# Kernel optimization log

Hardware: AMD Instinct MI355X
Metric: run time of the kernel (lower is better)

## Reference

```python
import jax, jax.numpy as jnp
import numpy as np

D_MODEL = 1024
D_FF = 4 * D_MODEL
NUM_EXPERTS = 8
TOP_K = 2
TOKENS = 4096


def setup_inputs() -> dict:
    key = jax.random.key(0)
    ks = jax.random.split(key, 8)
    s = 0.02
    x = jax.random.normal(ks[0], (TOKENS, D_MODEL), dtype=jnp.float32)
    Wg = jax.random.normal(ks[1], (D_MODEL, NUM_EXPERTS), dtype=jnp.float32) * s
    bg = jnp.zeros((NUM_EXPERTS,), dtype=jnp.float32)
    W1 = jax.random.normal(ks[2], (NUM_EXPERTS, D_MODEL, D_FF), dtype=jnp.float32) * s
    b1 = jnp.zeros((NUM_EXPERTS, D_FF), dtype=jnp.float32)
    W2 = jax.random.normal(ks[3], (NUM_EXPERTS, D_FF, D_MODEL), dtype=jnp.float32) * s
    b2 = jnp.zeros((NUM_EXPERTS, D_MODEL), dtype=jnp.float32)
    return {"x": x, "Wg": Wg, "bg": bg, "W1": W1, "b1": b1, "W2": W2, "b2": b2}


def reference(x, Wg, bg, W1, b1, W2, b2):
    # Gating: softmax over experts, select top-k indices per token.
    gate_scores = jax.nn.softmax(x @ Wg + bg, axis=-1)        # [T, E]
    _, top_k_idx = jax.lax.top_k(gate_scores, TOP_K)          # [T, K]
    # Binary combine mask: 1 where expert selected (top_k indices are distinct).
    # NOTE: original sums selected expert outputs WITHOUT gate weighting.
    mask = jnp.sum(jax.nn.one_hot(top_k_idx, NUM_EXPERTS, dtype=x.dtype), axis=1)  # [T, E]
    out = jnp.zeros_like(x)
    for e in range(NUM_EXPERTS):  # small fixed expert count
        h = jax.nn.relu(x @ W1[e] + b1[e])                    # [T, 4D]
        y = h @ W2[e] + b2[e]                                 # [T, D]
        out = out + mask[:, e:e + 1] * y
    return out
```

## Files before the change

kernel.cpp:

```cpp
#include <hip/hip_runtime.h>
#include <hip/hip_bf16.h>

#define T_TOKENS 4096
#define DM 1024
#define DF 4096
#define NE 8
#define MAXROWS 9216

typedef float f32x4 __attribute__((ext_vector_type(4)));
typedef short bf16x8 __attribute__((ext_vector_type(8)));

__device__ __forceinline__ unsigned short f2bf(float f) {
    union { float f; unsigned int u; } v; v.f = f;
    unsigned int r = v.u + 0x7fffu + ((v.u >> 16) & 1u);
    return (unsigned short)(r >> 16);
}

__device__ __forceinline__ void g2l16(const void* g, void* l) {
    __builtin_amdgcn_global_load_lds(
        (const __attribute__((address_space(1))) void*)g,
        (__attribute__((address_space(3))) void*)l, 16, 0, 0);
}

__global__ __launch_bounds__(256) void gate_kernel(
    const float* __restrict__ x, const float* __restrict__ Wg, const float* __restrict__ bg,
    int* __restrict__ counts, int* __restrict__ topk)
{
    int wave = threadIdx.x >> 6;
    int lane = threadIdx.x & 63;
    int t = blockIdx.x * 4 + wave;
    float acc[NE];
#pragma unroll
    for (int e = 0; e < NE; e++) acc[e] = 0.f;
    const float* xr = x + (size_t)t * DM;
#pragma unroll
    for (int i = 0; i < DM / 64; i++) {
        int d = lane + i * 64;
        float xv = xr[d];
        const float4* wg = (const float4*)(Wg + d * NE);
        float4 w0 = wg[0], w1 = wg[1];
        acc[0] += xv * w0.x; acc[1] += xv * w0.y; acc[2] += xv * w0.z; acc[3] += xv * w0.w;
        acc[4] += xv * w1.x; acc[5] += xv * w1.y; acc[6] += xv * w1.z; acc[7] += xv * w1.w;
    }
#pragma unroll
    for (int e = 0; e < NE; e++) {
#pragma unroll
        for (int off = 32; off > 0; off >>= 1)
            acc[e] += __shfl_down(acc[e], off);
    }
    if (lane == 0) {
        float lg[NE];
#pragma unroll
        for (int e = 0; e < NE; e++) lg[e] = acc[e] + bg[e];
        int b1i = 0; float b1v = lg[0];
        for (int e = 1; e < NE; e++) if (lg[e] > b1v) { b1v = lg[e]; b1i = e; }
        int b2i = -1; float b2v = -1e30f;
        for (int e = 0; e < NE; e++) {
            if (e == b1i) continue;
            if (b2i < 0 || lg[e] > b2v) { b2v = lg[e]; b2i = e; }
        }
        topk[t * 2 + 0] = b1i;
        topk[t * 2 + 1] = b2i;
        atomicAdd(&counts[b1i], 1);
        atomicAdd(&counts[b2i], 1);
    }
}

__global__ __launch_bounds__(256) void scatter_kernel(
    const int* __restrict__ counts, const int* __restrict__ topk,
    int* __restrict__ offsets, int* __restrict__ list)
{
    __shared__ int offs[NE + 1];
    __shared__ int cur[NE];
    if (threadIdx.x == 0) {
        int s = 0;
        for (int e = 0; e < NE; e++) {
            offs[e] = s; offsets[e] = s;
            s += (counts[e] + 127) & ~127;
        }
        offs[NE] = s; offsets[NE] = s;
    }
    if (threadIdx.x < NE) cur[threadIdx.x] = 0;
    __syncthreads();
    for (int i = threadIdx.x; i < T_TOKENS * 2; i += 256) {
        int e = topk[i];
        int pos = atomicAdd(&cur[e], 1);
        list[offs[e] + pos] = i >> 1;
    }
    __syncthreads();
    for (int e = 0; e < NE; e++) {
        int s = offs[e] + counts[e];
        int t = offs[e + 1];
        for (int i = s + threadIdx.x; i < t; i += 256) list[i] = -1;
    }
}

__global__ __launch_bounds__(256) void cvt_x_kernel(
    const float* __restrict__ x, unsigned short* __restrict__ xb)
{
    int i = (blockIdx.x * 256 + threadIdx.x) * 4;
    float4 v = *(const float4*)(x + i);
    unsigned short o[4] = { f2bf(v.x), f2bf(v.y), f2bf(v.z), f2bf(v.w) };
    *(uint2*)(xb + i) = *(const uint2*)o;
}

__global__ __launch_bounds__(256) void tr_cvt_kernel(
    const float* __restrict__ src, unsigned short* __restrict__ dst, int K, int N)
{
    const int e = blockIdx.z;
    src += (size_t)e * K * N;
    dst += (size_t)e * N * K;
    const int n0 = blockIdx.x * 64, k0 = blockIdx.y * 64;
    __shared__ unsigned short tile[64][68];
    const int t = threadIdx.x;
    const int tx = t & 63, ty = t >> 6;
#pragma unroll
    for (int r = 0; r < 16; r++) {
        int k = ty * 16 + r;
        tile[tx][k] = f2bf(src[(size_t)(k0 + k) * N + n0 + tx]);
    }
    __syncthreads();
    const int kx = (t & 15) * 4, ny = t >> 4;
#pragma unroll
    for (int r = 0; r < 4; r++) {
        int n = ny + r * 16;
        *(uint2*)(dst + (size_t)(n0 + n) * K + k0 + kx) = *(const uint2*)&tile[n][kx];
    }
}

__global__ __launch_bounds__(256) void gemm1_kernel(
    const unsigned short* __restrict__ xb, const unsigned short* __restrict__ W1T,
    const float* __restrict__ b1, const int* __restrict__ offsets,
    const int* __restrict__ list, unsigned short* __restrict__ H)
{
    const int total = offsets[NE];
    const int row0 = blockIdx.x * 128;
    if (row0 >= total) return;
    int e = 0;
    while (row0 >= offsets[e + 1]) e++;
    const int n0 = blockIdx.y * 128;

    __shared__ unsigned short Asm[128 * 32];
    __shared__ unsigned short Bsm[128 * 32];

    const int tid = threadIdx.x;
    const int w = tid >> 6, lane = tid & 63;
    const int quad = lane >> 4, l16 = lane & 15;
    const int wm = w >> 1, wn = w & 1;

    const int sr = lane >> 2;
    const int sc = (lane & 3) * 8;
    const int ra1 = 32 * w + sr, ra2 = ra1 + 16;
    int t1 = list[row0 + ra1]; if (t1 < 0) t1 = 0;
    int t2 = list[row0 + ra2]; if (t2 < 0) t2 = 0;
    const unsigned short* gA1 = xb + (size_t)t1 * DM + sc;
    const unsigned short* gA2 = xb + (size_t)t2 * DM + sc;
    const unsigned short* Wb = W1T + (size_t)e * DF * DM;
    const unsigned short* gB1 = Wb + (size_t)(n0 + 32 * w + sr) * DM + sc;
    const unsigned short* gB2 = gB1 + (size_t)16 * DM;
    unsigned short* lA1 = Asm + (2 * w) * 512;
    unsigned short* lA2 = Asm + (2 * w + 1) * 512;
    unsigned short* lB1 = Bsm + (2 * w) * 512;
    unsigned short* lB2 = Bsm + (2 * w + 1) * 512;

    f32x4 acc[4][4];
#pragma unroll
    for (int i = 0; i < 4; i++)
#pragma unroll
        for (int j = 0; j < 4; j++) acc[i][j] = (f32x4){0.f, 0.f, 0.f, 0.f};

    for (int kk = 0; kk < DM; kk += 32) {
        g2l16(gA1 + kk, lA1);
        g2l16(gA2 + kk, lA2);
        g2l16(gB1 + kk, lB1);
        g2l16(gB2 + kk, lB2);
        __syncthreads();
        bf16x8 af[4];
#pragma unroll
        for (int i = 0; i < 4; i++)
            af[i] = *(const bf16x8*)&Asm[(wm * 64 + i * 16 + l16) * 32 + quad * 8];
#pragma unroll
        for (int j = 0; j < 4; j++) {
            bf16x8 bf = *(const bf16x8*)&Bsm[(wn * 64 + j * 16 + l16) * 32 + quad * 8];
#pragma unroll
            for (int i = 0; i < 4; i++)
                acc[i][j] = __builtin_amdgcn_mfma_f32_16x16x32_bf16(af[i], bf, acc[i][j], 0, 0, 0);
        }
        __syncthreads();
    }

    const float* bias = b1 + e * DF;
#pragma unroll
    for (int j = 0; j < 4; j++) {
        int n = n0 + wn * 64 + j * 16 + l16;
        float bj = bias[n];
#pragma unroll
        for (int i = 0; i < 4; i++) {
            int row = row0 + wm * 64 + i * 16 + quad * 4;
#pragma unroll
            for (int r = 0; r < 4; r++) {
                float v = acc[i][j][r] + bj;
                v = fmaxf(v, 0.f);
                H[(size_t)(row + r) * DF + n] = f2bf(v);
            }
        }
    }
}

__global__ __launch_bounds__(256) void gemm2_kernel(
    const unsigned short* __restrict__ H, const unsigned short* __restrict__ W2T,
    const float* __restrict__ b2, const int* __restrict__ offsets,
    const int* __restrict__ list, float* __restrict__ out)
{
    const int total = offsets[NE];
    const int row0 = blockIdx.x * 128;
    if (row0 >= total) return;
    int e = 0;
    while (row0 >= offsets[e + 1]) e++;
    const int n0 = blockIdx.y * 128;

    __shared__ unsigned short Asm[128 * 32];
    __shared__ unsigned short Bsm[128 * 32];

    const int tid = threadIdx.x;
    const int w = tid >> 6, lane = tid & 63;
    const int quad = lane >> 4, l16 = lane & 15;
    const int wm = w >> 1, wn = w & 1;

    const int sr = lane >> 2;
    const int sc = (lane & 3) * 8;
    const unsigned short* gA1 = H + (size_t)(row0 + 32 * w + sr) * DF + sc;
    const unsigned short* gA2 = gA1 + (size_t)16 * DF;
    const unsigned short* Wb = W2T + (size_t)e * DM * DF;
    const unsigned short* gB1 = Wb + (size_t)(n0 + 32 * w + sr) * DF + sc;
    const unsigned short* gB2 = gB1 + (size_t)16 * DF;
    unsigned short* lA1 = Asm + (2 * w) * 512;
    unsigned short* lA2 = Asm + (2 * w + 1) * 512;
    unsigned short* lB1 = Bsm + (2 * w) * 512;
    unsigned short* lB2 = Bsm + (2 * w + 1) * 512;

    f32x4 acc[4][4];
#pragma unroll
    for (int i = 0; i < 4; i++)
#pragma unroll
        for (int j = 0; j < 4; j++) acc[i][j] = (f32x4){0.f, 0.f, 0.f, 0.f};

    for (int kk = 0; kk < DF; kk += 32) {
        g2l16(gA1 + kk, lA1);
        g2l16(gA2 + kk, lA2);
        g2l16(gB1 + kk, lB1);
        g2l16(gB2 + kk, lB2);
        __syncthreads();
        bf16x8 af[4];
#pragma unroll
        for (int i = 0; i < 4; i++)
            af[i] = *(const bf16x8*)&Asm[(wm * 64 + i * 16 + l16) * 32 + quad * 8];
#pragma unroll
        for (int j = 0; j < 4; j++) {
            bf16x8 bf = *(const bf16x8*)&Bsm[(wn * 64 + j * 16 + l16) * 32 + quad * 8];
#pragma unroll
            for (int i = 0; i < 4; i++)
                acc[i][j] = __builtin_amdgcn_mfma_f32_16x16x32_bf16(af[i], bf, acc[i][j], 0, 0, 0);
        }
        __syncthreads();
    }

    const float* bias = b2 + e * DM;
#pragma unroll
    for (int j = 0; j < 4; j++) {
        int n = n0 + wn * 64 + j * 16 + l16;
        float bj = bias[n];
#pragma unroll
        for (int i = 0; i < 4; i++) {
            int row = row0 + wm * 64 + i * 16 + quad * 4;
#pragma unroll
            for (int r = 0; r < 4; r++) {
                int tk = list[row + r];
                if (tk >= 0)
                    atomicAdd(&out[(size_t)tk * DM + n], acc[i][j][r] + bj);
            }
        }
    }
}

extern "C" void kernel_launch(void* const* d_in, const int* in_sizes, int n_in,
                              void* d_out, int out_size, void* d_ws, size_t ws_size,
                              hipStream_t stream)
{
    const float* x  = (const float*)d_in[0];
    const float* Wg = (const float*)d_in[1];
    const float* bg = (const float*)d_in[2];
    const float* W1 = (const float*)d_in[3];
    const float* b1 = (const float*)d_in[4];
    const float* W2 = (const float*)d_in[5];
    const float* b2 = (const float*)d_in[6];
    float* out = (float*)d_out;

    char* ws = (char*)d_ws;
    int* counts  = (int*)(ws + 0);
    int* offsets = (int*)(ws + 64);
    int* topk    = (int*)(ws + 256);
    int* list    = (int*)(ws + 33024);
    unsigned short* xb = (unsigned short*)(ws + (1u << 20));
    unsigned short* WT = (unsigned short*)(ws + (16u << 20));
    unsigned short* Hb = (unsigned short*)(ws + (80u << 20));

    hipMemsetAsync(counts, 0, NE * sizeof(int), stream);
    hipMemsetAsync(d_out, 0, (size_t)out_size * sizeof(float), stream);

    gate_kernel<<<T_TOKENS / 4, 256, 0, stream>>>(x, Wg, bg, counts, topk);
    scatter_kernel<<<1, 256, 0, stream>>>(counts, topk, offsets, list);
    cvt_x_kernel<<<T_TOKENS * DM / 1024, 256, 0, stream>>>(x, xb);

    tr_cvt_kernel<<<dim3(DF / 64, DM / 64, NE), 256, 0, stream>>>(W1, WT, DM, DF);
    gemm1_kernel<<<dim3(MAXROWS / 128, DF / 128), 256, 0, stream>>>(
        xb, WT, b1, offsets, list, Hb);

    tr_cvt_kernel<<<dim3(DM / 64, DF / 64, NE), 256, 0, stream>>>(W2, WT, DF, DM);
    gemm2_kernel<<<dim3(MAXROWS / 128, DM / 128), 256, 0, stream>>>(
        Hb, WT, b2, offsets, list, out);
}
```

Baseline: 683.5 us.

## Double-buffer LDS, XOR-swizzle tiles, and split-K the second expert GEMM

Both expert GEMM kernels now use two LDS buffers. The next K-slice's global-to-LDS loads are issued before the current slice's MFMAs, and one barrier per iteration replaces two, so load latency overlaps compute. The LDS column chunks are XOR-swizzled by row on both the write and read side, which is meant to cut bank conflicts on the bf16x8 fragment reads. gemm2 is split into two K halves along grid z, which doubles its block count for better occupancy; the bias is added only by the first half. The cost is twice the float atomicAdd traffic into the output and twice the LDS footprint per block.

```diff
diff --git a/kernel.cpp b/kernel.cpp
--- a/kernel.cpp
+++ b/kernel.cpp
@@ -140,8 +140,8 @@
     while (row0 >= offsets[e + 1]) e++;
     const int n0 = blockIdx.y * 128;
 
-    __shared__ unsigned short Asm[128 * 32];
-    __shared__ unsigned short Bsm[128 * 32];
+    __shared__ unsigned short Asm[2][4096];
+    __shared__ unsigned short Bsm[2][4096];
 
     const int tid = threadIdx.x;
     const int w = tid >> 6, lane = tid & 63;
@@ -149,7 +149,9 @@
     const int wm = w >> 1, wn = w & 1;
 
     const int sr = lane >> 2;
-    const int sc = (lane & 3) * 8;
+    const int sc = (((lane & 3) ^ ((sr >> 1) & 3))) * 8;
+    const int qx8 = (quad ^ ((l16 >> 1) & 3)) * 8;
+
     const int ra1 = 32 * w + sr, ra2 = ra1 + 16;
     int t1 = list[row0 + ra1]; if (t1 < 0) t1 = 0;
     int t2 = list[row0 + ra2]; if (t2 < 0) t2 = 0;
@@ -158,10 +160,10 @@
     const unsigned short* Wb = W1T + (size_t)e * DF * DM;
     const unsigned short* gB1 = Wb + (size_t)(n0 + 32 * w + sr) * DM + sc;
     const unsigned short* gB2 = gB1 + (size_t)16 * DM;
-    unsigned short* lA1 = Asm + (2 * w) * 512;
-    unsigned short* lA2 = Asm + (2 * w + 1) * 512;
-    unsigned short* lB1 = Bsm + (2 * w) * 512;
-    unsigned short* lB2 = Bsm + (2 * w + 1) * 512;
+    unsigned short* lA1 = &Asm[0][(2 * w) * 512];
+    unsigned short* lA2 = &Asm[0][(2 * w + 1) * 512];
+    unsigned short* lB1 = &Bsm[0][(2 * w) * 512];
+    unsigned short* lB2 = &Bsm[0][(2 * w + 1) * 512];
 
     f32x4 acc[4][4];
 #pragma unroll
@@ -169,25 +171,32 @@
 #pragma unroll
         for (int j = 0; j < 4; j++) acc[i][j] = (f32x4){0.f, 0.f, 0.f, 0.f};
 
+#define STAGE1(b, kk) do { \
+        g2l16(gA1 + (kk), lA1 + (b) * 4096); \
+        g2l16(gA2 + (kk), lA2 + (b) * 4096); \
+        g2l16(gB1 + (kk), lB1 + (b) * 4096); \
+        g2l16(gB2 + (kk), lB2 + (b) * 4096); } while (0)
+
+    STAGE1(0, 0);
+    __syncthreads();
+#pragma unroll 2
     for (int kk = 0; kk < DM; kk += 32) {
-        g2l16(gA1 + kk, lA1);
-        g2l16(gA2 + kk, lA2);
-        g2l16(gB1 + kk, lB1);
-        g2l16(gB2 + kk, lB2);
+        const int b = (kk >> 5) & 1;
+        if (kk + 32 < DM) STAGE1(b ^ 1, kk + 32);
+        bf16x8 af[4];
+#pragma unroll
+        for (int i = 0; i < 4; i++)
+            af[i] = *(const bf16x8*)&Asm[b][(wm * 64 + i * 16 + l16) * 32 + qx8];
+#pragma unroll
+        for (int j = 0; j < 4; j++) {
+            bf16x8 bfv = *(const bf16x8*)&Bsm[b][(wn * 64 + j * 16 + l16) * 32 + qx8];
+#pragma unroll
+            for (int i = 0; i < 4; i++)
+                acc[i][j] = __builtin_amdgcn_mfma_f32_16x16x32_bf16(af[i], bfv, acc[i][j], 0, 0, 0);
+        }
         __syncthreads();
-        bf16x8 af[4];
-#pragma unroll
-        for (int i = 0; i < 4; i++)
-            af[i] = *(const bf16x8*)&Asm[(wm * 64 + i * 16 + l16) * 32 + quad * 8];
-#pragma unroll
-        for (int j = 0; j < 4; j++) {
-            bf16x8 bf = *(const bf16x8*)&Bsm[(wn * 64 + j * 16 + l16) * 32 + quad * 8];
-#pragma unroll
-            for (int i = 0; i < 4; i++)
-                acc[i][j] = __builtin_amdgcn_mfma_f32_16x16x32_bf16(af[i], bf, acc[i][j], 0, 0, 0);
-        }
-        __syncthreads();
-    }
+    }
+#undef STAGE1
 
     const float* bias = b1 + e * DF;
 #pragma unroll
@@ -218,9 +227,11 @@
     int e = 0;
     while (row0 >= offsets[e + 1]) e++;
     const int n0 = blockIdx.y * 128;
-
-    __shared__ unsigned short Asm[128 * 32];
-    __shared__ unsigned short Bsm[128 * 32];
+    const int kz = blockIdx.z;
+    const int k0 = kz * (DF / 2);
+
+    __shared__ unsigned short Asm[2][4096];
+    __shared__ unsigned short Bsm[2][4096];
 
     const int tid = threadIdx.x;
     const int w = tid >> 6, lane = tid & 63;
@@ -228,16 +239,18 @@
     const int wm = w >> 1, wn = w & 1;
 
     const int sr = lane >> 2;
-    const int sc = (lane & 3) * 8;
-    const unsigned short* gA1 = H + (size_t)(row0 + 32 * w + sr) * DF + sc;
+    const int sc = (((lane & 3) ^ ((sr >> 1) & 3))) * 8;
+    const int qx8 = (quad ^ ((l16 >> 1) & 3)) * 8;
+
+    const unsigned short* gA1 = H + (size_t)(row0 + 32 * w + sr) * DF + k0 + sc;
     const unsigned short* gA2 = gA1 + (size_t)16 * DF;
     const unsigned short* Wb = W2T + (size_t)e * DM * DF;
-    const unsigned short* gB1 = Wb + (size_t)(n0 + 32 * w + sr) * DF + sc;
+    const unsigned short* gB1 = Wb + (size_t)(n0 + 32 * w + sr) * DF + k0 + sc;
     const unsigned short* gB2 = gB1 + (size_t)16 * DF;
-    unsigned short* lA1 = Asm + (2 * w) * 512;
-    unsigned short* lA2 = Asm + (2 * w + 1) * 512;
-    unsigned short* lB1 = Bsm + (2 * w) * 512;
-    unsigned short* lB2 = Bsm + (2 * w + 1) * 512;
+    unsigned short* lA1 = &Asm[0][(2 * w) * 512];
+    unsigned short* lA2 = &Asm[0][(2 * w + 1) * 512];
+    unsigned short* lB1 = &Bsm[0][(2 * w) * 512];
+    unsigned short* lB2 = &Bsm[0][(2 * w + 1) * 512];
 
     f32x4 acc[4][4];
 #pragma unroll
@@ -245,31 +258,38 @@
 #pragma unroll
         for (int j = 0; j < 4; j++) acc[i][j] = (f32x4){0.f, 0.f, 0.f, 0.f};
 
-    for (int kk = 0; kk < DF; kk += 32) {
-        g2l16(gA1 + kk, lA1);
-        g2l16(gA2 + kk, lA2);
-        g2l16(gB1 + kk, lB1);
-        g2l16(gB2 + kk, lB2);
+#define STAGE2(b, kk) do { \
+        g2l16(gA1 + (kk), lA1 + (b) * 4096); \
+        g2l16(gA2 + (kk), lA2 + (b) * 4096); \
+        g2l16(gB1 + (kk), lB1 + (b) * 4096); \
+        g2l16(gB2 + (kk), lB2 + (b) * 4096); } while (0)
+
+    STAGE2(0, 0);
+    __syncthreads();
+#pragma unroll 2
+    for (int kk = 0; kk < DF / 2; kk += 32) {
+        const int b = (kk >> 5) & 1;
+        if (kk + 32 < DF / 2) STAGE2(b ^ 1, kk + 32);
+        bf16x8 af[4];
+#pragma unroll
+        for (int i = 0; i < 4; i++)
+            af[i] = *(const bf16x8*)&Asm[b][(wm * 64 + i * 16 + l16) * 32 + qx8];
+#pragma unroll
+        for (int j = 0; j < 4; j++) {
+            bf16x8 bfv = *(const bf16x8*)&Bsm[b][(wn * 64 + j * 16 + l16) * 32 + qx8];
+#pragma unroll
+            for (int i = 0; i < 4; i++)
+                acc[i][j] = __builtin_amdgcn_mfma_f32_16x16x32_bf16(af[i], bfv, acc[i][j], 0, 0, 0);
+        }
         __syncthreads();
-        bf16x8 af[4];
-#pragma unroll
-        for (int i = 0; i < 4; i++)
-            af[i] = *(const bf16x8*)&Asm[(wm * 64 + i * 16 + l16) * 32 + quad * 8];
-#pragma unroll
-        for (int j = 0; j < 4; j++) {
-            bf16x8 bf = *(const bf16x8*)&Bsm[(wn * 64 + j * 16 + l16) * 32 + quad * 8];
-#pragma unroll
-            for (int i = 0; i < 4; i++)
-                acc[i][j] = __builtin_amdgcn_mfma_f32_16x16x32_bf16(af[i], bf, acc[i][j], 0, 0, 0);
-        }
-        __syncthreads();
-    }
+    }
+#undef STAGE2
 
     const float* bias = b2 + e * DM;
 #pragma unroll
     for (int j = 0; j < 4; j++) {
         int n = n0 + wn * 64 + j * 16 + l16;
-        float bj = bias[n];
+        float bj = (kz == 0) ? bias[n] : 0.f;
 #pragma unroll
         for (int i = 0; i < 4; i++) {
             int row = row0 + wm * 64 + i * 16 + quad * 4;
@@ -317,6 +337,6 @@
         xb, WT, b1, offsets, list, Hb);
 
     tr_cvt_kernel<<<dim3(DM / 64, DF / 64, NE), 256, 0, stream>>>(W2, WT, DF, DM);
-    gemm2_kernel<<<dim3(MAXROWS / 128, DM / 128), 256, 0, stream>>>(
+    gemm2_kernel<<<dim3(MAXROWS / 128, DM / 128, 2), 256, 0, stream>>>(
         Hb, WT, b2, offsets, list, out);
 }
```

Result: slower. 716.2 us (+4.8%).

## Swizzle LDS, double K-step per sync, stage GEMM1 epilogue, vectorize transpose loads

Applied to the files above, without the earlier changes.

Both grouped GEMMs now load two 32-wide K slices before each barrier pair, which halves the number of synchronizations. They also XOR-swizzle the LDS column placement so fragment reads avoid bank conflicts. GEMM1 writes its bf16 ReLU output into shared memory first and then stores full 16-byte rows to H instead of scattered 2-byte stores. The weight transpose-convert kernel reads float4 vectors instead of scalars. LDS use per block grows, which may reduce occupancy.

```diff
diff --git a/kernel.cpp b/kernel.cpp
--- a/kernel.cpp
+++ b/kernel.cpp
@@ -113,11 +113,16 @@
     const int n0 = blockIdx.x * 64, k0 = blockIdx.y * 64;
     __shared__ unsigned short tile[64][68];
     const int t = threadIdx.x;
-    const int tx = t & 63, ty = t >> 6;
-#pragma unroll
-    for (int r = 0; r < 16; r++) {
-        int k = ty * 16 + r;
-        tile[tx][k] = f2bf(src[(size_t)(k0 + k) * N + n0 + tx]);
+    const int c4 = (t & 15) * 4;
+    const int kr = t >> 4;
+#pragma unroll
+    for (int r = 0; r < 4; r++) {
+        int k = kr + r * 16;
+        float4 v = *(const float4*)(src + (size_t)(k0 + k) * N + n0 + c4);
+        tile[c4 + 0][k] = f2bf(v.x);
+        tile[c4 + 1][k] = f2bf(v.y);
+        tile[c4 + 2][k] = f2bf(v.z);
+        tile[c4 + 3][k] = f2bf(v.w);
     }
     __syncthreads();
     const int kx = (t & 15) * 4, ny = t >> 4;
@@ -140,8 +145,9 @@
     while (row0 >= offsets[e + 1]) e++;
     const int n0 = blockIdx.y * 128;
 
-    __shared__ unsigned short Asm[128 * 32];
-    __shared__ unsigned short Bsm[128 * 32];
+    __shared__ unsigned short smem[17408];
+    unsigned short* sA = smem;
+    unsigned short* sB = smem + 8192;
 
     const int tid = threadIdx.x;
     const int w = tid >> 6, lane = tid & 63;
@@ -149,7 +155,9 @@
     const int wm = w >> 1, wn = w & 1;
 
     const int sr = lane >> 2;
-    const int sc = (lane & 3) * 8;
+    const int sc = (((lane & 3) ^ ((sr >> 1) & 3))) * 8;
+    const int qx8 = (quad ^ ((l16 >> 1) & 3)) * 8;
+
     const int ra1 = 32 * w + sr, ra2 = ra1 + 16;
     int t1 = list[row0 + ra1]; if (t1 < 0) t1 = 0;
     int t2 = list[row0 + ra2]; if (t2 < 0) t2 = 0;
@@ -158,10 +166,6 @@
     const unsigned short* Wb = W1T + (size_t)e * DF * DM;
     const unsigned short* gB1 = Wb + (size_t)(n0 + 32 * w + sr) * DM + sc;
     const unsigned short* gB2 = gB1 + (size_t)16 * DM;
-    unsigned short* lA1 = Asm + (2 * w) * 512;
-    unsigned short* lA2 = Asm + (2 * w + 1) * 512;
-    unsigned short* lB1 = Bsm + (2 * w) * 512;
-    unsigned short* lB2 = Bsm + (2 * w + 1) * 512;
 
     f32x4 acc[4][4];
 #pragma unroll
@@ -169,41 +173,59 @@
 #pragma unroll
         for (int j = 0; j < 4; j++) acc[i][j] = (f32x4){0.f, 0.f, 0.f, 0.f};
 
-    for (int kk = 0; kk < DM; kk += 32) {
-        g2l16(gA1 + kk, lA1);
-        g2l16(gA2 + kk, lA2);
-        g2l16(gB1 + kk, lB1);
-        g2l16(gB2 + kk, lB2);
+#define STAGE1(h, kk) do { \
+        g2l16(gA1 + (kk), sA + (h) * 4096 + (2 * w) * 512); \
+        g2l16(gA2 + (kk), sA + (h) * 4096 + (2 * w + 1) * 512); \
+        g2l16(gB1 + (kk), sB + (h) * 4096 + (2 * w) * 512); \
+        g2l16(gB2 + (kk), sB + (h) * 4096 + (2 * w + 1) * 512); } while (0)
+
+    auto compute = [&](int h) {
+        bf16x8 af[4];
+#pragma unroll
+        for (int i = 0; i < 4; i++)
+            af[i] = *(const bf16x8*)&sA[h * 4096 + (wm * 64 + i * 16 + l16) * 32 + qx8];
+#pragma unroll
+        for (int j = 0; j < 4; j++) {
+            bf16x8 bfv = *(const bf16x8*)&sB[h * 4096 + (wn * 64 + j * 16 + l16) * 32 + qx8];
+#pragma unroll
+            for (int i = 0; i < 4; i++)
+                acc[i][j] = __builtin_amdgcn_mfma_f32_16x16x32_bf16(af[i], bfv, acc[i][j], 0, 0, 0);
+        }
+    };
+
+    for (int kk = 0; kk < DM; kk += 64) {
+        STAGE1(0, kk);
+        STAGE1(1, kk + 32);
         __syncthreads();
-        bf16x8 af[4];
-#pragma unroll
-        for (int i = 0; i < 4; i++)
-            af[i] = *(const bf16x8*)&Asm[(wm * 64 + i * 16 + l16) * 32 + quad * 8];
-#pragma unroll
-        for (int j = 0; j < 4; j++) {
-            bf16x8 bf = *(const bf16x8*)&Bsm[(wn * 64 + j * 16 + l16) * 32 + quad * 8];
-#pragma unroll
-            for (int i = 0; i < 4; i++)
-                acc[i][j] = __builtin_amdgcn_mfma_f32_16x16x32_bf16(af[i], bf, acc[i][j], 0, 0, 0);
-        }
+        compute(0);
+        compute(1);
         __syncthreads();
     }
+#undef STAGE1
 
     const float* bias = b1 + e * DF;
 #pragma unroll
     for (int j = 0; j < 4; j++) {
-        int n = n0 + wn * 64 + j * 16 + l16;
-        float bj = bias[n];
+        int nl = wn * 64 + j * 16 + l16;
+        float bj = bias[n0 + nl];
 #pragma unroll
         for (int i = 0; i < 4; i++) {
-            int row = row0 + wm * 64 + i * 16 + quad * 4;
+            int rl = wm * 64 + i * 16 + quad * 4;
 #pragma unroll
             for (int r = 0; r < 4; r++) {
                 float v = acc[i][j][r] + bj;
                 v = fmaxf(v, 0.f);
-                H[(size_t)(row + r) * DF + n] = f2bf(v);
+                smem[(rl + r) * 136 + nl] = f2bf(v);
             }
         }
+    }
+    __syncthreads();
+    const int rg = lane >> 4, cg = lane & 15;
+#pragma unroll
+    for (int i = 0; i < 8; i++) {
+        int rr = 32 * w + 4 * i + rg;
+        *(uint4*)&H[(size_t)(row0 + rr) * DF + n0 + cg * 8] =
+            *(const uint4*)&smem[rr * 136 + cg * 8];
     }
 }
 
@@ -219,8 +241,9 @@
     while (row0 >= offsets[e + 1]) e++;
     const int n0 = blockIdx.y * 128;
 
-    __shared__ unsigned short Asm[128 * 32];
-    __shared__ unsigned short Bsm[128 * 32];
+    __shared__ unsigned short smem[16384];
+    unsigned short* sA = smem;
+    unsigned short* sB = smem + 8192;
 
     const int tid = threadIdx.x;
     const int w = tid >> 6, lane = tid & 63;
@@ -228,16 +251,14 @@
     const int wm = w >> 1, wn = w & 1;
 
     const int sr = lane >> 2;
-    const int sc = (lane & 3) * 8;
+    const int sc = (((lane & 3) ^ ((sr >> 1) & 3))) * 8;
+    const int qx8 = (quad ^ ((l16 >> 1) & 3)) * 8;
+
     const unsigned short* gA1 = H + (size_t)(row0 + 32 * w + sr) * DF + sc;
     const unsigned short* gA2 = gA1 + (size_t)16 * DF;
     const unsigned short* Wb = W2T + (size_t)e * DM * DF;
     const unsigned short* gB1 = Wb + (size_t)(n0 + 32 * w + sr) * DF + sc;
     const unsigned short* gB2 = gB1 + (size_t)16 * DF;
-    unsigned short* lA1 = Asm + (2 * w) * 512;
-    unsigned short* lA2 = Asm + (2 * w + 1) * 512;
-    unsigned short* lB1 = Bsm + (2 * w) * 512;
-    unsigned short* lB2 = Bsm + (2 * w + 1) * 512;
 
     f32x4 acc[4][4];
 #pragma unroll
@@ -245,25 +266,35 @@
 #pragma unroll
         for (int j = 0; j < 4; j++) acc[i][j] = (f32x4){0.f, 0.f, 0.f, 0.f};
 
-    for (int kk = 0; kk < DF; kk += 32) {
-        g2l16(gA1 + kk, lA1);
-        g2l16(gA2 + kk, lA2);
-        g2l16(gB1 + kk, lB1);
-        g2l16(gB2 + kk, lB2);
+#define STAGE2(h, kk) do { \
+        g2l16(gA1 + (kk), sA + (h) * 4096 + (2 * w) * 512); \
+        g2l16(gA2 + (kk), sA + (h) * 4096 + (2 * w + 1) * 512); \
+        g2l16(gB1 + (kk), sB + (h) * 4096 + (2 * w) * 512); \
+        g2l16(gB2 + (kk), sB + (h) * 4096 + (2 * w + 1) * 512); } while (0)
+
+    auto compute = [&](int h) {
+        bf16x8 af[4];
+#pragma unroll
+        for (int i = 0; i < 4; i++)
+            af[i] = *(const bf16x8*)&sA[h * 4096 + (wm * 64 + i * 16 + l16) * 32 + qx8];
+#pragma unroll
+        for (int j = 0; j < 4; j++) {
+            bf16x8 bfv = *(const bf16x8*)&sB[h * 4096 + (wn * 64 + j * 16 + l16) * 32 + qx8];
+#pragma unroll
+            for (int i = 0; i < 4; i++)
+                acc[i][j] = __builtin_amdgcn_mfma_f32_16x16x32_bf16(af[i], bfv, acc[i][j], 0, 0, 0);
+        }
+    };
+
+    for (int kk = 0; kk < DF; kk += 64) {
+        STAGE2(0, kk);
+        STAGE2(1, kk + 32);
         __syncthreads();
-        bf16x8 af[4];
-#pragma unroll
-        for (int i = 0; i < 4; i++)
-            af[i] = *(const bf16x8*)&Asm[(wm * 64 + i * 16 + l16) * 32 + quad * 8];
-#pragma unroll
-        for (int j = 0; j < 4; j++) {
-            bf16x8 bf = *(const bf16x8*)&Bsm[(wn * 64 + j * 16 + l16) * 32 + quad * 8];
-#pragma unroll
-            for (int i = 0; i < 4; i++)
-                acc[i][j] = __builtin_amdgcn_mfma_f32_16x16x32_bf16(af[i], bf, acc[i][j], 0, 0, 0);
-        }
+        compute(0);
+        compute(1);
         __syncthreads();
     }
+#undef STAGE2
 
     const float* bias = b2 + e * DM;
 #pragma unroll
```

After: 692.1 us. Within noise of the previous version (+1.3%).
